# Kernel tuning notes

Hardware: AMD Instinct MI355X
Metric: run time of the kernel (lower is better)

Reference implementation:

```python
import jax, jax.numpy as jnp
import numpy as np


def setup_inputs() -> dict:
    key = jax.random.key(0)
    k1, k2, k3, k4, k5, k6 = jax.random.split(key, 6)
    B, V = 128, 128000
    logits = jax.random.normal(k1, (B, V), dtype=jnp.float32) * 2.0
    # keep temperatures away from 0 to avoid overflow in logits/temp
    temperatures = 0.7 + 0.6 * jax.random.uniform(k2, (B,), dtype=jnp.float32)
    top_ks = jax.random.randint(k3, (B,), 1, 1024, dtype=jnp.int32)
    top_ps = 0.7 + 0.29 * jax.random.uniform(k4, (B,), dtype=jnp.float32)
    min_ps = 0.02 * jax.random.uniform(k5, (B,), dtype=jnp.float32)
    # uniform variate for inverse-CDF multinomial sampling (one sample per row)
    u = jax.random.uniform(k6, (B, 1), dtype=jnp.float32)
    return {
        "logits": logits,
        "temperatures": temperatures,
        "top_ks": top_ks,
        "top_ps": top_ps,
        "min_ps": min_ps,
        "u": u,
    }


def reference(logits, temperatures, top_ks, top_ps, min_ps, u):
    """Faithful jax version of Sampler's torch-native sampling path:
    softmax(logits/T) -> descending sort -> top-k mask -> top-p mask
    (cumsum computed pre-mask, exactly as torch code) -> min-p mask ->
    multinomial sample (inverse CDF with provided uniform u) ->
    gather original token index. Also returns the renormalized filtered
    probs scattered back to vocab order (top_p_normalize_probs-style)."""
    B, V = logits.shape
    probs = jax.nn.softmax(logits / temperatures[:, None], axis=-1)  # [B, V]

    order = jnp.argsort(-probs, axis=-1)                     # descending indices
    probs_sort = jnp.take_along_axis(probs, order, axis=-1)  # [B, V] sorted desc
    probs_sum = jnp.cumsum(probs_sort, axis=-1)              # cumsum BEFORE masking

    pos = jnp.arange(V, dtype=jnp.int32)[None, :]
    # top-k: zero everything at rank >= top_k
    probs_sort = jnp.where(pos >= top_ks[:, None], 0.0, probs_sort)
    # top-p: zero where cumulative mass strictly before this token exceeds top_p
    probs_sort = jnp.where(probs_sum - probs_sort > top_ps[:, None], 0.0, probs_sort)
    # min-p: threshold relative to the max prob (rank-0 entry survives both masks)
    min_p_thr = probs_sort[:, :1] * min_ps[:, None]
    probs_sort = jnp.where(probs_sort < min_p_thr, 0.0, probs_sort)

    total = jnp.sum(probs_sort, axis=-1, keepdims=True)      # [B, 1]
    cdf = jnp.cumsum(probs_sort, axis=-1) / total            # normalized CDF
    # inverse-CDF sampling == torch.multinomial(probs_sort, 1)
    sampled_rank = jnp.clip(jnp.sum(cdf < u, axis=-1, keepdims=True), 0, V - 1)
    token_ids = jnp.take_along_axis(order, sampled_rank, axis=-1)[:, 0].astype(jnp.int32)

    # scatter renormalized filtered probs back to original vocab positions
    inv_order = jnp.argsort(order, axis=-1)
    norm_probs = jnp.take_along_axis(probs_sort / total, inv_order, axis=-1)
    return token_ids, norm_probs
```

## Files before the change

kernel.cpp:

```cpp
#include <hip/hip_runtime.h>
#include <stdint.h>
#include <math.h>

#define TPB 1024
#define NB 2048
#define SPLIT 4
#define LCAND 1536
#define CAND2 2048

typedef float vfloat4 __attribute__((ext_vector_type(4)));

__device__ __forceinline__ unsigned fkey(float f) {
    unsigned u = __float_as_uint(f);
    return (u & 0x80000000u) ? ~u : (u | 0x80000000u);
}
__device__ __forceinline__ float funkey(unsigned k) {
    unsigned u = (k & 0x80000000u) ? (k ^ 0x80000000u) : ~k;
    return __uint_as_float(u);
}

__device__ __forceinline__ void suffix_scan_2048(unsigned* h, unsigned* wscr, int tid)
{
    const int lane = tid & 63, w = tid >> 6;
    const int i0 = 2047 - 2 * tid;
    const int i1 = 2046 - 2 * tid;
    unsigned a = h[i0], b = h[i1];
    unsigned s = a + b;
    unsigned inc = s;
    #pragma unroll
    for (int d = 1; d < 64; d <<= 1) { unsigned o = __shfl_up(inc, d); if (lane >= d) inc += o; }
    if (lane == 63) wscr[w] = inc;
    __syncthreads();
    if (w == 0) {
        unsigned v = (lane < 16) ? wscr[lane] : 0u;
        unsigned vi = v;
        #pragma unroll
        for (int d = 1; d < 16; d <<= 1) { unsigned o = __shfl_up(vi, d); if (lane >= d) vi += o; }
        if (lane < 16) wscr[16 + lane] = vi - v;
    }
    __syncthreads();
    unsigned off = wscr[16 + w] + (inc - s);
    h[i0] = off + a;
    h[i1] = off + a + b;
    __syncthreads();
}

__global__ __launch_bounds__(TPB)
void k1_scan(const float* __restrict__ logits,
             const float* __restrict__ temps,
             const int* __restrict__ top_ks,
             float* __restrict__ out_probs,
             float* __restrict__ ws_ms,
             unsigned* __restrict__ ws_cnt,
             unsigned long long* __restrict__ ws_cand,
             int V, int Vq)
{
    const int blk = blockIdx.x;
    const int b = blk / SPLIT, s = blk % SPLIT;
    const int tid = threadIdx.x, lane = tid & 63, w = tid >> 6;
    const int start = s * Vq;
    const int len = min(Vq, V - start);
    const int slot = b * SPLIT + s;
    const float invT = 1.0f / temps[b];
    int K = top_ks[b];
    if (K < 1) K = 1;
    if (K > 1024) K = 1024;

    __shared__ unsigned sub[NB * 4];
    __shared__ unsigned hist[NB];
    __shared__ unsigned wscr[32];
    __shared__ float sm[TPB], ss[TPB];
    __shared__ unsigned cnt;
    __shared__ int b1loc;

    if (len <= 0) {
        if (tid == 0) {
            ws_ms[2 * slot] = -INFINITY; ws_ms[2 * slot + 1] = 0.0f; ws_cnt[slot] = 0;
        }
        return;
    }

    for (int i = tid; i < NB * 4; i += TPB) sub[i] = 0;
    if (tid == 0) cnt = 0;
    __syncthreads();

    const float* __restrict__ row = logits + (size_t)b * V + start;
    const vfloat4* __restrict__ row4 = (const vfloat4*)row;
    float* __restrict__ orow = out_probs + (size_t)b * V + start;
    vfloat4* __restrict__ orow4 = (vfloat4*)orow;
    const int L4 = len >> 2;
    const int c4 = tid & 3;
    const vfloat4 z4 = (vfloat4)0.0f;

    float m = -INFINITY, zsum = 0.0f;
    for (int i = tid; i < L4; i += TPB) {
        vfloat4 v = row4[i];
        __builtin_nontemporal_store(z4, &orow4[i]);
        #pragma unroll
        for (int j = 0; j < 4; ++j) {
            float lv = v[j];
            atomicAdd(&sub[((fkey(lv) >> 21) << 2) | c4], 1u);
            float y = lv * invT;
            if (y > m) { zsum = zsum * expf(m - y) + 1.0f; m = y; }
            else       { zsum += expf(y - m); }
        }
    }
    for (int i = (L4 << 2) + tid; i < len; i += TPB) {
        float lv = row[i];
        __builtin_nontemporal_store(0.0f, &orow[i]);
        atomicAdd(&sub[((fkey(lv) >> 21) << 2) | c4], 1u);
        float y = lv * invT;
        if (y > m) { zsum = zsum * expf(m - y) + 1.0f; m = y; }
        else       { zsum += expf(y - m); }
    }
    sm[tid] = m; ss[tid] = zsum;
    __syncthreads();
    for (int d = TPB >> 1; d > 0; d >>= 1) {
        if (tid < d) {
            float m1 = sm[tid], s1 = ss[tid];
            float m2 = sm[tid + d], s2 = ss[tid + d];
            float mm = fmaxf(m1, m2);
            float t1 = (s1 > 0.0f) ? s1 * expf(m1 - mm) : 0.0f;
            float t2 = (s2 > 0.0f) ? s2 * expf(m2 - mm) : 0.0f;
            ss[tid] = t1 + t2;
            sm[tid] = mm;
        }
        __syncthreads();
    }
    if (tid == 0) {
        ws_ms[2 * slot]     = sm[0];
        ws_ms[2 * slot + 1] = ss[0];
    }

    for (int j = tid; j < NB; j += TPB)
        hist[j] = sub[4 * j] + sub[4 * j + 1] + sub[4 * j + 2] + sub[4 * j + 3];
    __syncthreads();
    suffix_scan_2048(hist, wscr, tid);
    const unsigned Ku = (unsigned)K;
    const unsigned Ksearch = (Ku < (unsigned)len) ? Ku : (unsigned)len;
    for (int e = tid; e < NB; e += TPB) {
        unsigned Se = hist[e];
        unsigned Sn = (e < NB - 1) ? hist[e + 1] : 0u;
        if (Se >= Ksearch && Sn < Ksearch) b1loc = e;
    }
    __syncthreads();
    const unsigned Tloc = (unsigned)b1loc << 21;

    unsigned long long* gc = ws_cand + (size_t)slot * LCAND;
    for (int i = tid; i < L4; i += TPB) {
        vfloat4 v = row4[i];
        int base = start + (i << 2);
        #pragma unroll
        for (int j = 0; j < 4; ++j) {
            unsigned k = fkey(v[j]);
            if (k >= Tloc) {
                unsigned pos = atomicAdd(&cnt, 1u);
                if (pos < LCAND)
                    gc[pos] = ((unsigned long long)k << 32) |
                              (unsigned long long)(~(unsigned)(base + j));
            }
        }
    }
    for (int i = (L4 << 2) + tid; i < len; i += TPB) {
        unsigned k = fkey(row[i]);
        if (k >= Tloc) {
            unsigned pos = atomicAdd(&cnt, 1u);
            if (pos < LCAND)
                gc[pos] = ((unsigned long long)k << 32) |
                          (unsigned long long)(~(unsigned)(start + i));
        }
    }
    __syncthreads();
    if (tid == 0) ws_cnt[slot] = (cnt < LCAND) ? cnt : LCAND;
}

__global__ __launch_bounds__(TPB)
void k2_sample(const float* __restrict__ temps,
               const int* __restrict__ top_ks,
               const float* __restrict__ top_ps,
               const float* __restrict__ min_ps,
               const float* __restrict__ uvec,
               const float* __restrict__ ws_ms,
               const unsigned* __restrict__ ws_cnt,
               const unsigned long long* __restrict__ ws_cand,
               float* __restrict__ out_tok,
               float* __restrict__ out_probs,
               int V)
{
    const int b = blockIdx.x;
    const int tid = threadIdx.x, lane = tid & 63, w = tid >> 6;
    const float invT = 1.0f / temps[b];
    int K = top_ks[b];
    if (K < 1) K = 1;
    if (K > 1024) K = 1024;
    const float top_p = top_ps[b];
    const float min_p = min_ps[b];
    const float uval  = uvec[b];

    __shared__ unsigned sub[NB * 4];
    __shared__ unsigned hist[NB];
    __shared__ unsigned wscr[32];
    __shared__ __align__(16) unsigned long long cand[CAND2];
    __shared__ float sh_p[TPB], sh_c[TPB];
    __shared__ float fws[32];
    __shared__ unsigned cnt;
    __shared__ int sh_b1, sh_b2, sh_b3, sh_np, sh_nf;
    __shared__ unsigned sh_cab1, sh_cab2;

    float M = -INFINITY;
    #pragma unroll
    for (int q = 0; q < SPLIT; ++q) M = fmaxf(M, ws_ms[(size_t)(b * SPLIT + q) * 2]);
    float Z = 0.0f;
    #pragma unroll
    for (int q = 0; q < SPLIT; ++q) {
        float mm = ws_ms[(size_t)(b * SPLIT + q) * 2];
        float zz = ws_ms[(size_t)(b * SPLIT + q) * 2 + 1];
        if (zz > 0.0f) Z += zz * expf(mm - M);
    }
    int nlist[SPLIT];
    #pragma unroll
    for (int q = 0; q < SPLIT; ++q) nlist[q] = (int)ws_cnt[b * SPLIT + q];
    const unsigned Ku = (unsigned)K;
    const int c4 = tid & 3;

    for (int i = tid; i < NB * 4; i += TPB) sub[i] = 0;
    if (tid == 0) { cnt = 0; sh_b1 = 0; sh_b2 = 0; sh_b3 = 0; sh_cab1 = 0; sh_cab2 = 0; }
    __syncthreads();
    #pragma unroll
    for (int q = 0; q < SPLIT; ++q) {
        const unsigned long long* gc = ws_cand + (size_t)(b * SPLIT + q) * LCAND;
        for (int i = tid; i < nlist[q]; i += TPB)
            atomicAdd(&sub[(((unsigned)(gc[i] >> 32) >> 21) << 2) | c4], 1u);
    }
    __syncthreads();
    for (int j = tid; j < NB; j += TPB)
        hist[j] = sub[4 * j] + sub[4 * j + 1] + sub[4 * j + 2] + sub[4 * j + 3];
    __syncthreads();
    suffix_scan_2048(hist, wscr, tid);
    for (int e = tid; e < NB; e += TPB) {
        unsigned Se = hist[e];
        unsigned Sn = (e < NB - 1) ? hist[e + 1] : 0u;
        if (Se >= Ku && Sn < Ku) { sh_b1 = e; sh_cab1 = Sn; }
    }
    __syncthreads();
    const int b1 = sh_b1;
    const unsigned cab1 = sh_cab1;

    for (int i = tid; i < NB * 4; i += TPB) sub[i] = 0;
    __syncthreads();
    #pragma unroll
    for (int q = 0; q < SPLIT; ++q) {
        const unsigned long long* gc = ws_cand + (size_t)(b * SPLIT + q) * LCAND;
        for (int i = tid; i < nlist[q]; i += TPB) {
            unsigned k = (unsigned)(gc[i] >> 32);
            if ((int)(k >> 21) == b1)
                atomicAdd(&sub[(((k >> 10) & (NB - 1)) << 2) | c4], 1u);
        }
    }
    __syncthreads();
    for (int j = tid; j < NB; j += TPB)
        hist[j] = sub[4 * j] + sub[4 * j + 1] + sub[4 * j + 2] + sub[4 * j + 3];
    __syncthreads();
    suffix_scan_2048(hist, wscr, tid);
    for (int e = tid; e < NB; e += TPB) {
        unsigned Se = cab1 + hist[e];
        unsigned Sn = cab1 + ((e < NB - 1) ? hist[e + 1] : 0u);
        if (Se >= Ku && Sn < Ku) { sh_b2 = e; sh_cab2 = Sn; }
    }
    __syncthreads();
    const unsigned hi21 = ((unsigned)b1 << 11) | (unsigned)sh_b2;
    const unsigned cab2 = sh_cab2;

    for (int i = tid; i < NB * 4; i += TPB) sub[i] = 0;
    __syncthreads();
    #pragma unroll
    for (int q = 0; q < SPLIT; ++q) {
        const unsigned long long* gc = ws_cand + (size_t)(b * SPLIT + q) * LCAND;
        for (int i = tid; i < nlist[q]; i += TPB) {
            unsigned k = (unsigned)(gc[i] >> 32);
            if ((k >> 10) == hi21)
                atomicAdd(&sub[((k & 1023u) << 2) | c4], 1u);
        }
    }
    __syncthreads();
    for (int j = tid; j < NB; j += TPB)
        hist[j] = sub[4 * j] + sub[4 * j + 1] + sub[4 * j + 2] + sub[4 * j + 3];
    __syncthreads();
    suffix_scan_2048(hist, wscr, tid);
    for (int e = tid; e < 1024; e += TPB) {
        unsigned Se = cab2 + hist[e];
        unsigned Sn = cab2 + ((e < 1023) ? hist[e + 1] : 0u);
        if (Se >= Ku && Sn < Ku) sh_b3 = e;
    }
    __syncthreads();
    const unsigned Tkey = (hi21 << 10) | (unsigned)sh_b3;

    #pragma unroll
    for (int q = 0; q < SPLIT; ++q) {
        const unsigned long long* gc = ws_cand + (size_t)(b * SPLIT + q) * LCAND;
        for (int i = tid; i < nlist[q]; i += TPB) {
            unsigned long long e = gc[i];
            if ((unsigned)(e >> 32) >= Tkey) {
                unsigned pos = atomicAdd(&cnt, 1u);
                if (pos < CAND2) cand[pos] = e;
            }
        }
    }
    __syncthreads();
    int count = (cnt < (unsigned)CAND2) ? (int)cnt : CAND2;
    if (K > count) K = count;

    int n_sort = 1;
    while (n_sort < count) n_sort <<= 1;
    for (int i = tid; i < n_sort; i += TPB)
        if (i >= count) cand[i] = 0ull;
    __syncthreads();
    for (int kk = 2; kk <= n_sort; kk <<= 1) {
        for (int j = kk >> 1; j > 0; j >>= 1) {
            for (int i = tid; i < n_sort; i += TPB) {
                int ixj = i ^ j;
                if (ixj > i) {
                    unsigned long long a = cand[i];
                    unsigned long long c = cand[ixj];
                    bool up = (i & kk) == 0;
                    if (up ? (a < c) : (a > c)) { cand[i] = c; cand[ixj] = a; }
                }
            }
            __syncthreads();
        }
    }

    float pv = 0.0f;
    if (tid < K) {
        unsigned k = (unsigned)(cand[tid] >> 32);
        pv = expf(funkey(k) * invT - M) / Z;
    }
    float inc = pv;
    #pragma unroll
    for (int d = 1; d < 64; d <<= 1) { float o = __shfl_up(inc, d); if (lane >= d) inc += o; }
    if (lane == 63) fws[w] = inc;
    __syncthreads();
    if (w == 0) {
        float v = (lane < 16) ? fws[lane] : 0.0f;
        float vi = v;
        #pragma unroll
        for (int d = 1; d < 16; d <<= 1) { float o = __shfl_up(vi, d); if (lane >= d) vi += o; }
        if (lane < 16) fws[16 + lane] = vi - v;
    }
    __syncthreads();
    float cum = inc + fws[16 + w];
    sh_p[tid] = pv;
    sh_c[tid] = cum;
    if (tid == 0) sh_np = K;
    __syncthreads();

    if (tid < K) {
        float excl = cum - pv;
        if (excl > top_p) atomicMin(&sh_np, tid);
    }
    __syncthreads();
    int n1 = sh_np;
    float thr = sh_p[0] * min_p;
    if (tid == 0) sh_nf = n1;
    __syncthreads();
    if (tid < n1 && sh_p[tid] < thr) atomicMin(&sh_nf, tid);
    __syncthreads();
    int nf = sh_nf;
    float total = sh_c[nf - 1];

    int pred = (tid < nf) && ((sh_c[tid] / total) < uval);
    int rank = __syncthreads_count(pred);
    if (rank > nf - 1) rank = nf - 1;
    if (rank < 0) rank = 0;
    if (tid == 0) {
        unsigned idx = ~(unsigned)(cand[rank] & 0xFFFFFFFFull);
        out_tok[b] = (float)idx;
    }

    if (tid < nf) {
        unsigned idx = ~(unsigned)(cand[tid] & 0xFFFFFFFFull);
        out_probs[(size_t)b * V + idx] = sh_p[tid] / total;
    }
}

extern "C" void kernel_launch(void* const* d_in, const int* in_sizes, int n_in,
                              void* d_out, int out_size, void* d_ws, size_t ws_size,
                              hipStream_t stream) {
    const float* logits = (const float*)d_in[0];
    const float* temps  = (const float*)d_in[1];
    const int*   top_ks = (const int*)d_in[2];
    const float* top_ps = (const float*)d_in[3];
    const float* min_ps = (const float*)d_in[4];
    const float* u      = (const float*)d_in[5];
    const int B = in_sizes[1];
    const int V = in_sizes[0] / B;
    float* out_tok   = (float*)d_out;
    float* out_probs = out_tok + B;

    int Vq = (((V + SPLIT - 1) / SPLIT) + 3) & ~3;

    char* ws = (char*)d_ws;
    size_t off = 0;
    auto take = [&](size_t bytes) { char* p = ws + off; off = (off + bytes + 255) & ~(size_t)255; return p; };
    float*              ws_ms   = (float*)take((size_t)B * SPLIT * 2 * sizeof(float));
    unsigned*           ws_cnt  = (unsigned*)take((size_t)B * SPLIT * sizeof(unsigned));
    unsigned long long* ws_cand = (unsigned long long*)take((size_t)B * SPLIT * LCAND * sizeof(unsigned long long));
    (void)ws_size;

    k1_scan<<<dim3(SPLIT * B), dim3(TPB), 0, stream>>>(
        logits, temps, top_ks, out_probs, ws_ms, ws_cnt, ws_cand, V, Vq);
    k2_sample<<<dim3(B), dim3(TPB), 0, stream>>>(
        temps, top_ks, top_ps, min_ps, u, ws_ms, ws_cnt, ws_cand,
        out_tok, out_probs, V);
}
```

Before: 172.9 us.

## Single-pass candidate selection via sampled threshold, fixed-max softmax, fallback path

The first kernel now estimates a top-k cutoff from a histogram over the first 4096 elements. It then does a single pass over the row that fuses the output zeroing, a softmax sum using a fixed shift and exp2, a max, and candidate collection with batched atomics. Per-element histogram atomics and the online rescaled softmax are gone. The second kernel checks for candidate overflow and softmax overflow risk and falls back to a full-row recompute when either occurs. It sorts candidates with a bucketed insertion sort when buckets are small and uses bitonic sort otherwise. The sampled cutoff depends on the input distribution, and the fallback path is expensive.

After: 166.1 us. -3.9%, faster.

```diff
diff --git a/kernel.cpp b/kernel.cpp
--- a/kernel.cpp
+++ b/kernel.cpp
@@ -5,10 +5,13 @@
 #define TPB 1024
 #define NB 2048
 #define SPLIT 4
-#define LCAND 1536
+#define LCAND 2560
 #define CAND2 2048
+#define PS 4096
+#define L2E 1.44269504088896f
 
 typedef float vfloat4 __attribute__((ext_vector_type(4)));
+typedef unsigned long long ull;
 
 __device__ __forceinline__ unsigned fkey(float f) {
     unsigned u = __float_as_uint(f);
@@ -17,6 +20,9 @@
 __device__ __forceinline__ float funkey(unsigned k) {
     unsigned u = (k & 0x80000000u) ? (k ^ 0x80000000u) : ~k;
     return __uint_as_float(u);
+}
+__device__ __forceinline__ ull packkv(unsigned k, unsigned idx) {
+    return ((ull)k << 32) | (ull)(~idx);
 }
 
 __device__ __forceinline__ void suffix_scan_2048(unsigned* h, unsigned* wscr, int tid)
@@ -51,8 +57,9 @@
              const int* __restrict__ top_ks,
              float* __restrict__ out_probs,
              float* __restrict__ ws_ms,
+             unsigned* __restrict__ ws_cut,
              unsigned* __restrict__ ws_cnt,
-             unsigned long long* __restrict__ ws_cand,
+             ull* __restrict__ ws_cand,
              int V, int Vq)
 {
     const int blk = blockIdx.x;
@@ -60,28 +67,26 @@
     const int tid = threadIdx.x, lane = tid & 63, w = tid >> 6;
     const int start = s * Vq;
     const int len = min(Vq, V - start);
-    const int slot = b * SPLIT + s;
+    const int slot = blk;
     const float invT = 1.0f / temps[b];
-    int K = top_ks[b];
-    if (K < 1) K = 1;
-    if (K > 1024) K = 1024;
-
-    __shared__ unsigned sub[NB * 4];
+    int K = top_ks[b]; K = max(K, 1); K = min(K, 1024);
+
     __shared__ unsigned hist[NB];
-    __shared__ unsigned wscr[32];
-    __shared__ float sm[TPB], ss[TPB];
+    __shared__ unsigned uscr[32];
+    __shared__ float fred[32];
     __shared__ unsigned cnt;
-    __shared__ int b1loc;
+    __shared__ int bstar;
 
     if (len <= 0) {
         if (tid == 0) {
-            ws_ms[2 * slot] = -INFINITY; ws_ms[2 * slot + 1] = 0.0f; ws_cnt[slot] = 0;
+            ws_ms[4*slot] = -1e30f; ws_ms[4*slot+1] = 0.0f; ws_ms[4*slot+2] = -1e30f;
+            ws_cut[slot] = 0u; ws_cnt[slot] = 0u;
         }
         return;
     }
 
-    for (int i = tid; i < NB * 4; i += TPB) sub[i] = 0;
-    if (tid == 0) cnt = 0;
+    for (int i = tid; i < NB; i += TPB) hist[i] = 0;
+    if (tid == 0) { cnt = 0; bstar = 0; }
     __syncthreads();
 
     const float* __restrict__ row = logits + (size_t)b * V + start;
@@ -89,100 +94,103 @@
     float* __restrict__ orow = out_probs + (size_t)b * V + start;
     vfloat4* __restrict__ orow4 = (vfloat4*)orow;
     const int L4 = len >> 2;
-    const int c4 = tid & 3;
+
+    const int nps = min(len, PS);
+    float m0 = -1e30f;
+    for (int i = tid; i < nps; i += TPB) {
+        float lv = row[i];
+        m0 = fmaxf(m0, lv);
+        atomicAdd(&hist[fkey(lv) >> 21], 1u);
+    }
+    #pragma unroll
+    for (int d = 32; d > 0; d >>= 1) m0 = fmaxf(m0, __shfl_down(m0, d));
+    if (lane == 0) fred[w] = m0;
+    __syncthreads();
+    if (tid == 0) {
+        float mm = fred[0];
+        for (int j = 1; j < 16; ++j) mm = fmaxf(mm, fred[j]);
+        fred[16] = mm;
+    }
+    __syncthreads();
+    const float m0max = fred[16];
+
+    suffix_scan_2048(hist, uscr, tid);
+    unsigned TGT = (unsigned)((K * 13) / 64 + 16);
+    if (TGT > (unsigned)nps) TGT = (unsigned)nps;
+    for (int e = tid; e < NB; e += TPB) {
+        unsigned Se = hist[e];
+        unsigned Sn = (e < NB - 1) ? hist[e + 1] : 0u;
+        if (Se >= TGT && Sn < TGT) bstar = e;
+    }
+    __syncthreads();
+    const unsigned cutkey = (unsigned)bstar << 21;
+    const float cutval = funkey(cutkey);
+
+    const float ca = invT * L2E;
+    const float cb = -m0max * invT * L2E;
+
+    float z = 0.0f, mb = -1e30f;
+    ull* gc = ws_cand + (size_t)slot * LCAND;
     const vfloat4 z4 = (vfloat4)0.0f;
 
-    float m = -INFINITY, zsum = 0.0f;
     for (int i = tid; i < L4; i += TPB) {
         vfloat4 v = row4[i];
         __builtin_nontemporal_store(z4, &orow4[i]);
-        #pragma unroll
-        for (int j = 0; j < 4; ++j) {
-            float lv = v[j];
-            atomicAdd(&sub[((fkey(lv) >> 21) << 2) | c4], 1u);
-            float y = lv * invT;
-            if (y > m) { zsum = zsum * expf(m - y) + 1.0f; m = y; }
-            else       { zsum += expf(y - m); }
+        float x0 = v[0], x1 = v[1], x2 = v[2], x3 = v[3];
+        z += exp2f(fmaf(x0, ca, cb)) + exp2f(fmaf(x1, ca, cb))
+           + exp2f(fmaf(x2, ca, cb)) + exp2f(fmaf(x3, ca, cb));
+        mb = fmaxf(mb, fmaxf(fmaxf(x0, x1), fmaxf(x2, x3)));
+        bool c0 = x0 >= cutval, c1 = x1 >= cutval, c2 = x2 >= cutval, c3 = x3 >= cutval;
+        if (c0 | c1 | c2 | c3) {
+            int n = (int)c0 + (int)c1 + (int)c2 + (int)c3;
+            unsigned base = atomicAdd(&cnt, (unsigned)n);
+            unsigned bi = (unsigned)(start + (i << 2));
+            if (c0) { if (base < LCAND) gc[base] = packkv(fkey(x0), bi + 0); base++; }
+            if (c1) { if (base < LCAND) gc[base] = packkv(fkey(x1), bi + 1); base++; }
+            if (c2) { if (base < LCAND) gc[base] = packkv(fkey(x2), bi + 2); base++; }
+            if (c3) { if (base < LCAND) gc[base] = packkv(fkey(x3), bi + 3); base++; }
         }
     }
     for (int i = (L4 << 2) + tid; i < len; i += TPB) {
         float lv = row[i];
         __builtin_nontemporal_store(0.0f, &orow[i]);
-        atomicAdd(&sub[((fkey(lv) >> 21) << 2) | c4], 1u);
-        float y = lv * invT;
-        if (y > m) { zsum = zsum * expf(m - y) + 1.0f; m = y; }
-        else       { zsum += expf(y - m); }
-    }
-    sm[tid] = m; ss[tid] = zsum;
-    __syncthreads();
-    for (int d = TPB >> 1; d > 0; d >>= 1) {
-        if (tid < d) {
-            float m1 = sm[tid], s1 = ss[tid];
-            float m2 = sm[tid + d], s2 = ss[tid + d];
-            float mm = fmaxf(m1, m2);
-            float t1 = (s1 > 0.0f) ? s1 * expf(m1 - mm) : 0.0f;
-            float t2 = (s2 > 0.0f) ? s2 * expf(m2 - mm) : 0.0f;
-            ss[tid] = t1 + t2;
-            sm[tid] = mm;
-        }
-        __syncthreads();
-    }
+        z += exp2f(fmaf(lv, ca, cb));
+        mb = fmaxf(mb, lv);
+        if (lv >= cutval) {
+            unsigned base = atomicAdd(&cnt, 1u);
+            if (base < LCAND) gc[base] = packkv(fkey(lv), (unsigned)(start + i));
+        }
+    }
+    __syncthreads();
+    #pragma unroll
+    for (int d = 32; d > 0; d >>= 1) {
+        z += __shfl_down(z, d);
+        mb = fmaxf(mb, __shfl_down(mb, d));
+    }
+    if (lane == 0) { fred[w] = z; fred[16 + w] = mb; }
+    __syncthreads();
     if (tid == 0) {
-        ws_ms[2 * slot]     = sm[0];
-        ws_ms[2 * slot + 1] = ss[0];
-    }
-
-    for (int j = tid; j < NB; j += TPB)
-        hist[j] = sub[4 * j] + sub[4 * j + 1] + sub[4 * j + 2] + sub[4 * j + 3];
-    __syncthreads();
-    suffix_scan_2048(hist, wscr, tid);
-    const unsigned Ku = (unsigned)K;
-    const unsigned Ksearch = (Ku < (unsigned)len) ? Ku : (unsigned)len;
-    for (int e = tid; e < NB; e += TPB) {
-        unsigned Se = hist[e];
-        unsigned Sn = (e < NB - 1) ? hist[e + 1] : 0u;
-        if (Se >= Ksearch && Sn < Ksearch) b1loc = e;
-    }
-    __syncthreads();
-    const unsigned Tloc = (unsigned)b1loc << 21;
-
-    unsigned long long* gc = ws_cand + (size_t)slot * LCAND;
-    for (int i = tid; i < L4; i += TPB) {
-        vfloat4 v = row4[i];
-        int base = start + (i << 2);
-        #pragma unroll
-        for (int j = 0; j < 4; ++j) {
-            unsigned k = fkey(v[j]);
-            if (k >= Tloc) {
-                unsigned pos = atomicAdd(&cnt, 1u);
-                if (pos < LCAND)
-                    gc[pos] = ((unsigned long long)k << 32) |
-                              (unsigned long long)(~(unsigned)(base + j));
-            }
-        }
-    }
-    for (int i = (L4 << 2) + tid; i < len; i += TPB) {
-        unsigned k = fkey(row[i]);
-        if (k >= Tloc) {
-            unsigned pos = atomicAdd(&cnt, 1u);
-            if (pos < LCAND)
-                gc[pos] = ((unsigned long long)k << 32) |
-                          (unsigned long long)(~(unsigned)(start + i));
-        }
-    }
-    __syncthreads();
-    if (tid == 0) ws_cnt[slot] = (cnt < LCAND) ? cnt : LCAND;
+        float zz = 0.0f, mm = -1e30f;
+        for (int j = 0; j < 16; ++j) { zz += fred[j]; mm = fmaxf(mm, fred[16 + j]); }
+        ws_ms[4*slot + 0] = m0max * invT;
+        ws_ms[4*slot + 1] = zz;
+        ws_ms[4*slot + 2] = mm * invT;
+        ws_cut[slot] = cutkey;
+        ws_cnt[slot] = cnt;
+    }
 }
 
 __global__ __launch_bounds__(TPB)
-void k2_sample(const float* __restrict__ temps,
+void k2_sample(const float* __restrict__ logits,
+               const float* __restrict__ temps,
                const int* __restrict__ top_ks,
                const float* __restrict__ top_ps,
                const float* __restrict__ min_ps,
                const float* __restrict__ uvec,
                const float* __restrict__ ws_ms,
+               const unsigned* __restrict__ ws_cut,
                const unsigned* __restrict__ ws_cnt,
-               const unsigned long long* __restrict__ ws_cand,
+               const ull* __restrict__ ws_cand,
                float* __restrict__ out_tok,
                float* __restrict__ out_probs,
                int V)
@@ -190,150 +198,274 @@
     const int b = blockIdx.x;
     const int tid = threadIdx.x, lane = tid & 63, w = tid >> 6;
     const float invT = 1.0f / temps[b];
-    int K = top_ks[b];
-    if (K < 1) K = 1;
-    if (K > 1024) K = 1024;
-    const float top_p = top_ps[b];
-    const float min_p = min_ps[b];
-    const float uval  = uvec[b];
-
-    __shared__ unsigned sub[NB * 4];
-    __shared__ unsigned hist[NB];
-    __shared__ unsigned wscr[32];
-    __shared__ __align__(16) unsigned long long cand[CAND2];
-    __shared__ float sh_p[TPB], sh_c[TPB];
+    int Korig = top_ks[b]; Korig = max(Korig, 1); Korig = min(Korig, 1024);
+    const unsigned Ku = (unsigned)Korig;
+    const float top_p = top_ps[b], min_p = min_ps[b], uval = uvec[b];
+
+    __shared__ __align__(16) char smem[53504];
+    ull*            cand  = (ull*)(smem);
+    ull*            cand2 = (ull*)(smem + 16384);
+    unsigned*       hist  = (unsigned*)(smem + 32768);
+    unsigned short* cnts  = (unsigned short*)(smem + 41216);
+    float*          sh_p  = (float*)(smem + 45312);
+    float*          sh_c  = (float*)(smem + 49408);
+    __shared__ unsigned uscr[32];
     __shared__ float fws[32];
-    __shared__ unsigned cnt;
-    __shared__ int sh_b1, sh_b2, sh_b3, sh_np, sh_nf;
-    __shared__ unsigned sh_cab1, sh_cab2;
-
-    float M = -INFINITY;
-    #pragma unroll
-    for (int q = 0; q < SPLIT; ++q) M = fmaxf(M, ws_ms[(size_t)(b * SPLIT + q) * 2]);
+    __shared__ unsigned scnt;
+    __shared__ int sh_i1, sh_i2;
+    __shared__ unsigned sh_u1;
+
+    float Cy[SPLIT], zq[SPLIT], Mbyq[SPLIT];
+    unsigned cutq[SPLIT], cntq[SPLIT];
+    #pragma unroll
+    for (int q = 0; q < SPLIT; ++q) {
+        int sl = b * SPLIT + q;
+        Cy[q] = ws_ms[4*sl]; zq[q] = ws_ms[4*sl+1]; Mbyq[q] = ws_ms[4*sl+2];
+        cutq[q] = ws_cut[sl]; cntq[q] = ws_cnt[sl];
+    }
+    float Y = -1e30f;
+    #pragma unroll
+    for (int q = 0; q < SPLIT; ++q) Y = fmaxf(Y, Cy[q]);
     float Z = 0.0f;
     #pragma unroll
+    for (int q = 0; q < SPLIT; ++q)
+        if (zq[q] > 0.0f) Z += zq[q] * exp2f((Cy[q] - Y) * L2E);
+
+    bool fb = false;
+    #pragma unroll
     for (int q = 0; q < SPLIT; ++q) {
-        float mm = ws_ms[(size_t)(b * SPLIT + q) * 2];
-        float zz = ws_ms[(size_t)(b * SPLIT + q) * 2 + 1];
-        if (zz > 0.0f) Z += zz * expf(mm - M);
-    }
-    int nlist[SPLIT];
-    #pragma unroll
-    for (int q = 0; q < SPLIT; ++q) nlist[q] = (int)ws_cnt[b * SPLIT + q];
-    const unsigned Ku = (unsigned)K;
-    const int c4 = tid & 3;
-
-    for (int i = tid; i < NB * 4; i += TPB) sub[i] = 0;
-    if (tid == 0) { cnt = 0; sh_b1 = 0; sh_b2 = 0; sh_b3 = 0; sh_cab1 = 0; sh_cab2 = 0; }
-    __syncthreads();
-    #pragma unroll
-    for (int q = 0; q < SPLIT; ++q) {
-        const unsigned long long* gc = ws_cand + (size_t)(b * SPLIT + q) * LCAND;
-        for (int i = tid; i < nlist[q]; i += TPB)
-            atomicAdd(&sub[(((unsigned)(gc[i] >> 32) >> 21) << 2) | c4], 1u);
-    }
-    __syncthreads();
-    for (int j = tid; j < NB; j += TPB)
-        hist[j] = sub[4 * j] + sub[4 * j + 1] + sub[4 * j + 2] + sub[4 * j + 3];
-    __syncthreads();
-    suffix_scan_2048(hist, wscr, tid);
-    for (int e = tid; e < NB; e += TPB) {
-        unsigned Se = hist[e];
-        unsigned Sn = (e < NB - 1) ? hist[e + 1] : 0u;
-        if (Se >= Ku && Sn < Ku) { sh_b1 = e; sh_cab1 = Sn; }
-    }
-    __syncthreads();
-    const int b1 = sh_b1;
-    const unsigned cab1 = sh_cab1;
-
-    for (int i = tid; i < NB * 4; i += TPB) sub[i] = 0;
-    __syncthreads();
-    #pragma unroll
-    for (int q = 0; q < SPLIT; ++q) {
-        const unsigned long long* gc = ws_cand + (size_t)(b * SPLIT + q) * LCAND;
-        for (int i = tid; i < nlist[q]; i += TPB) {
-            unsigned k = (unsigned)(gc[i] >> 32);
-            if ((int)(k >> 21) == b1)
-                atomicAdd(&sub[(((k >> 10) & (NB - 1)) << 2) | c4], 1u);
-        }
-    }
-    __syncthreads();
-    for (int j = tid; j < NB; j += TPB)
-        hist[j] = sub[4 * j] + sub[4 * j + 1] + sub[4 * j + 2] + sub[4 * j + 3];
-    __syncthreads();
-    suffix_scan_2048(hist, wscr, tid);
-    for (int e = tid; e < NB; e += TPB) {
-        unsigned Se = cab1 + hist[e];
-        unsigned Sn = cab1 + ((e < NB - 1) ? hist[e + 1] : 0u);
-        if (Se >= Ku && Sn < Ku) { sh_b2 = e; sh_cab2 = Sn; }
-    }
-    __syncthreads();
-    const unsigned hi21 = ((unsigned)b1 << 11) | (unsigned)sh_b2;
-    const unsigned cab2 = sh_cab2;
-
-    for (int i = tid; i < NB * 4; i += TPB) sub[i] = 0;
-    __syncthreads();
-    #pragma unroll
-    for (int q = 0; q < SPLIT; ++q) {
-        const unsigned long long* gc = ws_cand + (size_t)(b * SPLIT + q) * LCAND;
-        for (int i = tid; i < nlist[q]; i += TPB) {
-            unsigned k = (unsigned)(gc[i] >> 32);
-            if ((k >> 10) == hi21)
-                atomicAdd(&sub[((k & 1023u) << 2) | c4], 1u);
-        }
-    }
-    __syncthreads();
-    for (int j = tid; j < NB; j += TPB)
-        hist[j] = sub[4 * j] + sub[4 * j + 1] + sub[4 * j + 2] + sub[4 * j + 3];
-    __syncthreads();
-    suffix_scan_2048(hist, wscr, tid);
-    for (int e = tid; e < 1024; e += TPB) {
-        unsigned Se = cab2 + hist[e];
-        unsigned Sn = cab2 + ((e < 1023) ? hist[e + 1] : 0u);
-        if (Se >= Ku && Sn < Ku) sh_b3 = e;
-    }
-    __syncthreads();
-    const unsigned Tkey = (hi21 << 10) | (unsigned)sh_b3;
-
-    #pragma unroll
-    for (int q = 0; q < SPLIT; ++q) {
-        const unsigned long long* gc = ws_cand + (size_t)(b * SPLIT + q) * LCAND;
-        for (int i = tid; i < nlist[q]; i += TPB) {
-            unsigned long long e = gc[i];
-            if ((unsigned)(e >> 32) >= Tkey) {
-                unsigned pos = atomicAdd(&cnt, 1u);
-                if (pos < CAND2) cand[pos] = e;
-            }
-        }
-    }
-    __syncthreads();
-    int count = (cnt < (unsigned)CAND2) ? (int)cnt : CAND2;
-    if (K > count) K = count;
-
-    int n_sort = 1;
-    while (n_sort < count) n_sort <<= 1;
-    for (int i = tid; i < n_sort; i += TPB)
-        if (i >= count) cand[i] = 0ull;
-    __syncthreads();
-    for (int kk = 2; kk <= n_sort; kk <<= 1) {
-        for (int j = kk >> 1; j > 0; j >>= 1) {
-            for (int i = tid; i < n_sort; i += TPB) {
-                int ixj = i ^ j;
-                if (ixj > i) {
-                    unsigned long long a = cand[i];
-                    unsigned long long c = cand[ixj];
-                    bool up = (i & kk) == 0;
-                    if (up ? (a < c) : (a > c)) { cand[i] = c; cand[ixj] = a; }
+        if (cntq[q] > (unsigned)LCAND) fb = true;
+        if (Mbyq[q] - Cy[q] > 60.0f) fb = true;
+    }
+    unsigned cutmax = 0;
+    #pragma unroll
+    for (int q = 0; q < SPLIT; ++q) cutmax = max(cutmax, cutq[q]);
+
+    unsigned Tkey = 0;
+    int count = 0;
+
+    if (!fb) {
+        for (int i = tid; i < NB; i += TPB) hist[i] = 0;
+        if (tid == 0) { sh_i1 = -1; sh_i2 = -1; }
+        __syncthreads();
+        #pragma unroll
+        for (int q = 0; q < SPLIT; ++q) {
+            const ull* gc = ws_cand + (size_t)(b * SPLIT + q) * LCAND;
+            int nl = min((int)cntq[q], LCAND);
+            for (int i = tid; i < nl; i += TPB)
+                atomicAdd(&hist[(unsigned)(gc[i] >> 32) >> 21], 1u);
+        }
+        __syncthreads();
+        suffix_scan_2048(hist, uscr, tid);
+        for (int e = tid; e < NB; e += TPB) {
+            unsigned Se = hist[e], Sn = (e < NB-1) ? hist[e+1] : 0u;
+            if (Se >= Ku && Sn < Ku) { sh_i1 = e; sh_u1 = Sn; }
+        }
+        __syncthreads();
+        int b1 = sh_i1;
+        unsigned cab = sh_u1;
+        if (b1 < 0) fb = true;
+        else {
+            for (int i = tid; i < NB; i += TPB) hist[i] = 0;
+            __syncthreads();
+            #pragma unroll
+            for (int q = 0; q < SPLIT; ++q) {
+                const ull* gc = ws_cand + (size_t)(b * SPLIT + q) * LCAND;
+                int nl = min((int)cntq[q], LCAND);
+                for (int i = tid; i < nl; i += TPB) {
+                    unsigned k = (unsigned)(gc[i] >> 32);
+                    if ((int)(k >> 21) == b1) atomicAdd(&hist[(k >> 10) & (NB - 1)], 1u);
                 }
             }
             __syncthreads();
-        }
+            suffix_scan_2048(hist, uscr, tid);
+            for (int e = tid; e < NB; e += TPB) {
+                unsigned Se = cab + hist[e];
+                unsigned Sn = cab + ((e < NB-1) ? hist[e+1] : 0u);
+                if (Se >= Ku && Sn < Ku) sh_i2 = e;
+            }
+            __syncthreads();
+            if (sh_i2 < 0) fb = true;
+            else {
+                Tkey = ((unsigned)b1 << 21) | ((unsigned)sh_i2 << 10);
+                if (Tkey < cutmax) fb = true;
+            }
+        }
+    }
+    if (!fb) {
+        if (tid == 0) scnt = 0;
+        __syncthreads();
+        #pragma unroll
+        for (int q = 0; q < SPLIT; ++q) {
+            const ull* gc = ws_cand + (size_t)(b * SPLIT + q) * LCAND;
+            int nl = min((int)cntq[q], LCAND);
+            for (int i = tid; i < nl; i += TPB) {
+                ull e = gc[i];
+                if ((unsigned)(e >> 32) >= Tkey) {
+                    unsigned pos = atomicAdd(&scnt, 1u);
+                    if (pos < CAND2) cand[pos] = e;
+                }
+            }
+        }
+        __syncthreads();
+        if (scnt > (unsigned)CAND2 || scnt < Ku) fb = true;
+        else count = (int)scnt;
+    }
+
+    if (fb) {
+        const float* __restrict__ row = logits + (size_t)b * V;
+        float m = -1e30f, z = 0.0f;
+        for (int i = tid; i < V; i += TPB) {
+            float y = row[i] * invT;
+            float nm = fmaxf(m, y);
+            z = z * exp2f((m - nm) * L2E) + exp2f((y - nm) * L2E);
+            m = nm;
+        }
+        sh_p[tid] = m; sh_c[tid] = z;
+        __syncthreads();
+        for (int d = TPB >> 1; d > 0; d >>= 1) {
+            if (tid < d) {
+                float m1 = sh_p[tid], z1 = sh_c[tid];
+                float m2 = sh_p[tid + d], z2 = sh_c[tid + d];
+                float mm = fmaxf(m1, m2);
+                sh_c[tid] = z1 * exp2f((m1 - mm) * L2E) + z2 * exp2f((m2 - mm) * L2E);
+                sh_p[tid] = mm;
+            }
+            __syncthreads();
+        }
+        Y = sh_p[0]; Z = sh_c[0];
+        __syncthreads();
+        for (int i = tid; i < NB; i += TPB) hist[i] = 0;
+        __syncthreads();
+        for (int i = tid; i < V; i += TPB) atomicAdd(&hist[fkey(row[i]) >> 21], 1u);
+        __syncthreads();
+        suffix_scan_2048(hist, uscr, tid);
+        for (int e = tid; e < NB; e += TPB) {
+            unsigned Se = hist[e], Sn = (e < NB-1) ? hist[e+1] : 0u;
+            if (Se >= Ku && Sn < Ku) { sh_i1 = e; sh_u1 = Sn; }
+        }
+        __syncthreads();
+        int b1 = sh_i1;
+        unsigned cab = sh_u1;
+        for (int i = tid; i < NB; i += TPB) hist[i] = 0;
+        __syncthreads();
+        for (int i = tid; i < V; i += TPB) {
+            unsigned k = fkey(row[i]);
+            if ((int)(k >> 21) == b1) atomicAdd(&hist[(k >> 10) & (NB - 1)], 1u);
+        }
+        __syncthreads();
+        suffix_scan_2048(hist, uscr, tid);
+        for (int e = tid; e < NB; e += TPB) {
+            unsigned Se = cab + hist[e];
+            unsigned Sn = cab + ((e < NB-1) ? hist[e+1] : 0u);
+            if (Se >= Ku && Sn < Ku) sh_i2 = e;
+        }
+        __syncthreads();
+        Tkey = ((unsigned)b1 << 21) | ((unsigned)sh_i2 << 10);
+        if (tid == 0) scnt = 0;
+        __syncthreads();
+        for (int i = tid; i < V; i += TPB) {
+            unsigned k = fkey(row[i]);
+            if (k >= Tkey) {
+                unsigned pos = atomicAdd(&scnt, 1u);
+                if (pos < CAND2) cand[pos] = packkv(k, (unsigned)i);
+            }
+        }
+        __syncthreads();
+        count = (scnt < (unsigned)CAND2) ? (int)scnt : CAND2;
+    }
+
+    int K = min(Korig, count);
+
+    unsigned mk = 0;
+    for (int i = tid; i < count; i += TPB) mk = max(mk, (unsigned)(cand[i] >> 32));
+    #pragma unroll
+    for (int d = 32; d > 0; d >>= 1) mk = max(mk, __shfl_down(mk, d));
+    if (lane == 0) uscr[w] = mk;
+    __syncthreads();
+    if (tid == 0) {
+        unsigned m2 = 0;
+        for (int j = 0; j < 16; ++j) m2 = max(m2, uscr[j]);
+        uscr[16] = m2;
+    }
+    __syncthreads();
+    const unsigned maxkey = uscr[16];
+    const unsigned range = maxkey - Tkey;
+    int shift = 0;
+    while ((range >> shift) > (NB - 1)) shift++;
+
+    for (int i = tid; i <= NB; i += TPB) hist[i] = 0;
+    __syncthreads();
+    for (int i = tid; i < count; i += TPB)
+        atomicAdd(&hist[((unsigned)(cand[i] >> 32) - Tkey) >> shift], 1u);
+    __syncthreads();
+    unsigned mc = 0;
+    for (int i = tid; i < NB; i += TPB) {
+        unsigned h = hist[i];
+        cnts[i] = (unsigned short)h;
+        mc = max(mc, h);
+    }
+    #pragma unroll
+    for (int d = 32; d > 0; d >>= 1) mc = max(mc, __shfl_down(mc, d));
+    if (lane == 0) uscr[w] = mc;
+    __syncthreads();
+    if (tid == 0) {
+        unsigned m2 = 0;
+        for (int j = 0; j < 16; ++j) m2 = max(m2, uscr[j]);
+        uscr[17] = m2;
+    }
+    __syncthreads();
+    const bool use_bitonic = (uscr[17] > 48u);
+    ull* srt;
+    if (!use_bitonic) {
+        suffix_scan_2048(hist, uscr, tid);
+        for (int i = tid; i < count; i += TPB) {
+            ull v = cand[i];
+            unsigned bin = ((unsigned)(v >> 32) - Tkey) >> shift;
+            unsigned pos = atomicAdd(&hist[bin + 1], 1u);
+            cand2[pos] = v;
+        }
+        __syncthreads();
+        for (int bn = tid; bn < NB; bn += TPB) {
+            int c = (int)cnts[bn];
+            if (c >= 2) {
+                int st = (int)hist[bn + 1] - c;
+                for (int x = 1; x < c; ++x) {
+                    ull key = cand2[st + x];
+                    int y = x - 1;
+                    while (y >= 0 && cand2[st + y] < key) { cand2[st + y + 1] = cand2[st + y]; --y; }
+                    cand2[st + y + 1] = key;
+                }
+            }
+        }
+        __syncthreads();
+        srt = cand2;
+    } else {
+        int n_sort = 1;
+        while (n_sort < count) n_sort <<= 1;
+        for (int i = tid; i < n_sort; i += TPB)
+            if (i >= count) cand[i] = 0ull;
+        __syncthreads();
+        for (int kk = 2; kk <= n_sort; kk <<= 1) {
+            for (int j = kk >> 1; j > 0; j >>= 1) {
+                for (int i = tid; i < n_sort; i += TPB) {
+                    int ixj = i ^ j;
+                    if (ixj > i) {
+                        ull a = cand[i], c = cand[ixj];
+                        bool up = (i & kk) == 0;
+                        if (up ? (a < c) : (a > c)) { cand[i] = c; cand[ixj] = a; }
+                    }
+                }
+                __syncthreads();
+            }
+        }
+        srt = cand;
     }
 
     float pv = 0.0f;
     if (tid < K) {
-        unsigned k = (unsigned)(cand[tid] >> 32);
-        pv = expf(funkey(k) * invT - M) / Z;
+        unsigned k = (unsigned)(srt[tid] >> 32);
+        pv = exp2f((funkey(k) * invT - Y) * L2E) / Z;
     }
     float inc = pv;
     #pragma unroll
@@ -351,34 +483,32 @@
     float cum = inc + fws[16 + w];
     sh_p[tid] = pv;
     sh_c[tid] = cum;
-    if (tid == 0) sh_np = K;
+    if (tid == 0) sh_i1 = K;
     __syncthreads();
 
     if (tid < K) {
         float excl = cum - pv;
-        if (excl > top_p) atomicMin(&sh_np, tid);
-    }
-    __syncthreads();
-    int n1 = sh_np;
+        if (excl > top_p) atomicMin(&sh_i1, tid);
+    }
+    __syncthreads();
+    int n1 = sh_i1;
     float thr = sh_p[0] * min_p;
-    if (tid == 0) sh_nf = n1;
-    __syncthreads();
-    if (tid < n1 && sh_p[tid] < thr) atomicMin(&sh_nf, tid);
-    __syncthreads();
-    int nf = sh_nf;
+    if (tid == 0) sh_i2 = n1;
+    __syncthreads();
+    if (tid < n1 && sh_p[tid] < thr) atomicMin(&sh_i2, tid);
+    __syncthreads();
+    int nf = sh_i2;
     float total = sh_c[nf - 1];
 
     int pred = (tid < nf) && ((sh_c[tid] / total) < uval);
     int rank = __syncthreads_count(pred);
     if (rank > nf - 1) rank = nf - 1;
     if (rank < 0) rank = 0;
-    if (tid == 0) {
-        unsigned idx = ~(unsigned)(cand[rank] & 0xFFFFFFFFull);
-        out_tok[b] = (float)idx;
-    }
+    if (tid == 0)
+        out_tok[b] = (float)(~(unsigned)(srt[rank] & 0xFFFFFFFFull));
 
     if (tid < nf) {
-        unsigned idx = ~(unsigned)(cand[tid] & 0xFFFFFFFFull);
+        unsigned idx = ~(unsigned)(srt[tid] & 0xFFFFFFFFull);
         out_probs[(size_t)b * V + idx] = sh_p[tid] / total;
     }
 }
@@ -402,14 +532,15 @@
     char* ws = (char*)d_ws;
     size_t off = 0;
     auto take = [&](size_t bytes) { char* p = ws + off; off = (off + bytes + 255) & ~(size_t)255; return p; };
-    float*              ws_ms   = (float*)take((size_t)B * SPLIT * 2 * sizeof(float));
-    unsigned*           ws_cnt  = (unsigned*)take((size_t)B * SPLIT * sizeof(unsigned));
-    unsigned long long* ws_cand = (unsigned long long*)take((size_t)B * SPLIT * LCAND * sizeof(unsigned long long));
+    float*    ws_ms   = (float*)take((size_t)B * SPLIT * 4 * sizeof(float));
+    unsigned* ws_cut  = (unsigned*)take((size_t)B * SPLIT * sizeof(unsigned));
+    unsigned* ws_cnt  = (unsigned*)take((size_t)B * SPLIT * sizeof(unsigned));
+    ull*      ws_cand = (ull*)take((size_t)B * SPLIT * LCAND * sizeof(ull));
     (void)ws_size;
 
     k1_scan<<<dim3(SPLIT * B), dim3(TPB), 0, stream>>>(
-        logits, temps, top_ks, out_probs, ws_ms, ws_cnt, ws_cand, V, Vq);
+        logits, temps, top_ks, out_probs, ws_ms, ws_cut, ws_cnt, ws_cand, V, Vq);
     k2_sample<<<dim3(B), dim3(TPB), 0, stream>>>(
-        temps, top_ks, top_ps, min_ps, u, ws_ms, ws_cnt, ws_cand,
+        logits, temps, top_ks, top_ps, min_ps, u, ws_ms, ws_cut, ws_cnt, ws_cand,
         out_tok, out_probs, V);
 }
```
